# Kernel tuning notes

Measured on AMD Instinct MI355X. Metric: run time of the kernel, lower is better.

The kernel has to match this reference:

```python
import jax, jax.numpy as jnp
import numpy as np

N_NODES = 50000
N_EDGES = 1600000
IN_FEATS = 64
EDGE_INFEAT = 32
HID_FEATS = 128
OUT_FEATS = 4


def setup_inputs() -> dict:
    key = jax.random.key(0)
    ks = jax.random.split(key, 8)
    h = jax.random.normal(ks[0], (N_NODES, IN_FEATS), dtype=jnp.float32)
    edge_feat = jax.random.normal(ks[1], (N_EDGES, EDGE_INFEAT), dtype=jnp.float32)
    src = jax.random.randint(ks[2], (N_EDGES,), 0, N_NODES, dtype=jnp.int32)
    dst = jax.random.randint(ks[3], (N_EDGES,), 0, N_NODES, dtype=jnp.int32)
    cat_dim = 2 * IN_FEATS + EDGE_INFEAT
    # Kaiming-ish scaled weights (nn.Linear default scale ~ 1/sqrt(fan_in))
    W1_w = jax.random.normal(ks[4], (cat_dim, HID_FEATS), dtype=jnp.float32) / np.sqrt(cat_dim)
    W1_b = jax.random.normal(ks[5], (HID_FEATS,), dtype=jnp.float32) * 0.01
    W2_w = jax.random.normal(ks[6], (HID_FEATS, OUT_FEATS), dtype=jnp.float32) / np.sqrt(HID_FEATS)
    W2_b = jax.random.normal(ks[7], (OUT_FEATS,), dtype=jnp.float32) * 0.01
    return {"h": h, "edge_feat": edge_feat, "src": src, "dst": dst,
            "W1_w": W1_w, "W1_b": W1_b, "W2_w": W2_w, "W2_b": W2_b}


def reference(h, edge_feat, src, dst, W1_w, W1_b, W2_w, W2_b):
    # Gather per-edge src/dst node features.  [E, in_feats]
    h_u = jnp.take(h, src, axis=0)
    h_v = jnp.take(h, dst, axis=0)
    # Avoid materializing the [E, 2*in+edge] concat: split the GEMM over the
    # three weight blocks (same math as cat -> Linear).
    Wu = W1_w[:IN_FEATS]            # [in_feats, hid]
    Wv = W1_w[IN_FEATS:2 * IN_FEATS]
    We = W1_w[2 * IN_FEATS:]        # [edge_infeat, hid]
    hid = h_u @ Wu + h_v @ Wv + edge_feat @ We + W1_b  # [E, hid]
    hid = jax.nn.relu(hid)
    return hid @ W2_w + W2_b  # [E, 4]
```

## Files before the change

### kernel.cpp

```cpp
#include <hip/hip_runtime.h>
#include <hip/hip_bf16.h>

#define N_NODES 50000
#define N_EDGES 1600000
#define IN_F 64
#define E_F 32
#define HID 128
#define OUT_F 4

typedef __attribute__((ext_vector_type(4))) float f32x4;
typedef __attribute__((ext_vector_type(8))) short short8;
typedef __attribute__((ext_vector_type(4))) int i32x4;

__device__ inline short f2bf(float f) {
  union { float f; unsigned u; } v; v.f = f;
  unsigned r = v.u + 0x7FFFu + ((v.u >> 16) & 1u);
  return (short)(r >> 16);
}
__device__ inline float bf2f(short s) {
  union { unsigned u; float f; } v; v.u = ((unsigned)(unsigned short)s) << 16;
  return v.f;
}

__global__ __launch_bounds__(256) void node_pre(const float* __restrict__ h,
                                                const float* __restrict__ W1,
                                                short* __restrict__ P) {
  __shared__ float Wl[128 * 128];
  __shared__ float hl[4][64];
  const int tid = threadIdx.x;
  for (int i = tid; i < 128 * 128; i += 256) {
    const int k = i >> 7, j = i & 127;
    Wl[k * 128 + ((j & 15) * 8 + (j >> 4))] = W1[i];
  }

  const int o    = tid & 127;
  const int half = tid >> 7;

  int n0 = blockIdx.x * 98;
  int n1 = min(n0 + 98, N_NODES);
  __syncthreads();

  for (int nb = n0; nb < n1; nb += 4) {
    const int nn = min(4, n1 - nb);
    __syncthreads();
    {
      const int m = tid >> 6, k = tid & 63;
      if (m < nn) hl[m][k] = h[(nb + m) * IN_F + k];
    }
    __syncthreads();
    float acc[4] = {0.f, 0.f, 0.f, 0.f};
#pragma unroll
    for (int k = 0; k < 64; ++k) {
      const float w = Wl[(half * 64 + k) * 128 + o];
#pragma unroll
      for (int m = 0; m < 4; ++m) acc[m] = fmaf(hl[m][k], w, acc[m]);
    }
#pragma unroll
    for (int m = 0; m < 4; ++m)
      if (m < nn) P[(size_t)(nb + m) * 256 + half * 128 + o] = f2bf(acc[m]);
  }
}

#define TPB 8
__global__ __launch_bounds__(256) void edge_mlp(
    const float* __restrict__ ef, const int* __restrict__ src,
    const int* __restrict__ dst, const float* __restrict__ W1,
    const float* __restrict__ b1, const float* __restrict__ W2,
    const float* __restrict__ b2, const short* __restrict__ P,
    float* __restrict__ out) {
  __shared__ __align__(16) short Elds[64 * 32];

  const int tid  = threadIdx.x;
  const int lane = tid & 63;
  const int wid  = tid >> 6;
  const int col  = lane & 15;
  const int rowg = lane >> 4;

  short8 bfrag[8];
#pragma unroll
  for (int t = 0; t < 8; ++t) {
#pragma unroll
    for (int i = 0; i < 8; ++i) {
      const float f = W1[(2 * IN_F + rowg * 8 + i) * HID + t * 16 + col];
      bfrag[t][i] = f2bf(f);
    }
  }
  float b1r[8];
  f32x4 w2r[8];
#pragma unroll
  for (int t = 0; t < 8; ++t) {
    b1r[t] = b1[t * 16 + col];
    w2r[t] = ((const f32x4*)W2)[t * 16 + col];
  }
  const f32x4 b2r = *((const f32x4*)b2);

  for (int tt = 0; tt < TPB; ++tt) {
    const int e0 = (blockIdx.x * TPB + tt) * 64;

    const int ebase = e0 + wid * 16 + rowg * 4;
    const i32x4 se = __builtin_nontemporal_load((const i32x4*)(src + ebase));
    const i32x4 de = __builtin_nontemporal_load((const i32x4*)(dst + ebase));

    const f32x4* efv = (const f32x4*)(ef + (size_t)e0 * E_F);
    const f32x4 a0 = __builtin_nontemporal_load(efv + tid * 2);
    const f32x4 a1 = __builtin_nontemporal_load(efv + tid * 2 + 1);
    short8 pk;
#pragma unroll
    for (int i = 0; i < 4; ++i) pk[i] = f2bf(a0[i]);
#pragma unroll
    for (int i = 0; i < 4; ++i) pk[4 + i] = f2bf(a1[i]);
    __syncthreads();
    ((short8*)Elds)[tid] = pk;
    __syncthreads();

    const short8 af = ((short8*)Elds)[(wid * 16 + col) * 4 + rowg];
    f32x4 acc[8];
#pragma unroll
    for (int t = 0; t < 8; ++t)
      acc[t] = __builtin_amdgcn_mfma_f32_16x16x32_bf16(
          af, bfrag[t], (f32x4){0.f, 0.f, 0.f, 0.f}, 0, 0, 0);

    const int sidx[4] = {se.x, se.y, se.z, se.w};
    const int didx[4] = {de.x, de.y, de.z, de.w};
    short8 lu[4], lv[4];
#pragma unroll
    for (int q = 0; q < 4; ++q) {
      lu[q] = *(const short8*)(P + (size_t)sidx[q] * 256 + col * 8);
      lv[q] = *(const short8*)(P + (size_t)didx[q] * 256 + 128 + col * 8);
    }
    f32x4 part[4] = {(f32x4){0,0,0,0}, (f32x4){0,0,0,0},
                     (f32x4){0,0,0,0}, (f32x4){0,0,0,0}};
#pragma unroll
    for (int q = 0; q < 4; ++q) {
#pragma unroll
      for (int t = 0; t < 8; ++t) {
        float hid = acc[t][q] + bf2f(lu[q][t]) + bf2f(lv[q][t]) + b1r[t];
        hid = fmaxf(hid, 0.f);
#pragma unroll
        for (int o = 0; o < 4; ++o)
          part[q][o] = fmaf(hid, w2r[t][o], part[q][o]);
      }
    }

#pragma unroll
    for (int q = 0; q < 4; ++q) {
#pragma unroll
      for (int o = 0; o < 4; ++o) {
        float v = part[q][o];
        v += __shfl_xor(v, 1);
        v += __shfl_xor(v, 2);
        v += __shfl_xor(v, 4);
        v += __shfl_xor(v, 8);
        part[q][o] = v + b2r[o];
      }
    }
    if (col == 0) {
#pragma unroll
      for (int q = 0; q < 4; ++q)
        __builtin_nontemporal_store(part[q], (f32x4*)out + ebase + q);
    }
  }
}

extern "C" void kernel_launch(void* const* d_in, const int* in_sizes, int n_in,
                              void* d_out, int out_size, void* d_ws, size_t ws_size,
                              hipStream_t stream) {
  const float* h   = (const float*)d_in[0];
  const float* ef  = (const float*)d_in[1];
  const int*   src = (const int*)d_in[2];
  const int*   dst = (const int*)d_in[3];
  const float* W1  = (const float*)d_in[4];
  const float* b1  = (const float*)d_in[5];
  const float* W2  = (const float*)d_in[6];
  const float* b2  = (const float*)d_in[7];
  float* out = (float*)d_out;
  short* P   = (short*)d_ws;

  hipLaunchKernelGGL(node_pre, dim3(512), dim3(256), 0, stream, h, W1, P);
  hipLaunchKernelGGL(edge_mlp, dim3(N_EDGES / (64 * TPB)), dim3(256), 0, stream,
                     ef, src, dst, W1, b1, W2, b2, P, out);
}
```

Baseline: 510.7 us.

## Drop LDS staging in edge and node kernels; load MFMA fragments directly per wave

The edge kernel no longer stages edge features through shared memory with two block barriers per tile. Each wave now owns independent 16-edge tiles and loads its bf16 A-fragment straight from global memory in MFMA layout. The node precompute kernel keeps its weight column in 64 registers instead of LDS, uses more blocks with 49 nodes each, and computes one node at a time. This removes barrier stalls and LDS traffic, at the cost of less coalesced edge-feature loads (32-byte strided rows) and higher register pressure in node_pre.

```diff
diff --git a/kernel.cpp b/kernel.cpp
--- a/kernel.cpp
+++ b/kernel.cpp
@@ -25,51 +25,38 @@
 __global__ __launch_bounds__(256) void node_pre(const float* __restrict__ h,
                                                 const float* __restrict__ W1,
                                                 short* __restrict__ P) {
-  __shared__ float Wl[128 * 128];
-  __shared__ float hl[4][64];
-  const int tid = threadIdx.x;
-  for (int i = tid; i < 128 * 128; i += 256) {
-    const int k = i >> 7, j = i & 127;
-    Wl[k * 128 + ((j & 15) * 8 + (j >> 4))] = W1[i];
-  }
-
+  const int tid  = threadIdx.x;
   const int o    = tid & 127;
   const int half = tid >> 7;
+  const int j    = (o & 7) * 16 + (o >> 3);
 
-  int n0 = blockIdx.x * 98;
-  int n1 = min(n0 + 98, N_NODES);
-  __syncthreads();
+  float wreg[64];
+#pragma unroll
+  for (int k = 0; k < 64; ++k) wreg[k] = W1[(half * 64 + k) * 128 + j];
 
-  for (int nb = n0; nb < n1; nb += 4) {
-    const int nn = min(4, n1 - nb);
-    __syncthreads();
-    {
-      const int m = tid >> 6, k = tid & 63;
-      if (m < nn) hl[m][k] = h[(nb + m) * IN_F + k];
+  const int n0 = blockIdx.x * 49;
+  const int n1 = min(n0 + 49, N_NODES);
+  for (int n = n0; n < n1; ++n) {
+    const float* __restrict__ hrow = h + (size_t)n * IN_F;
+    float a0 = 0.f, a1 = 0.f, a2 = 0.f, a3 = 0.f;
+#pragma unroll
+    for (int k = 0; k < 64; k += 4) {
+      a0 = fmaf(hrow[k    ], wreg[k    ], a0);
+      a1 = fmaf(hrow[k + 1], wreg[k + 1], a1);
+      a2 = fmaf(hrow[k + 2], wreg[k + 2], a2);
+      a3 = fmaf(hrow[k + 3], wreg[k + 3], a3);
     }
-    __syncthreads();
-    float acc[4] = {0.f, 0.f, 0.f, 0.f};
-#pragma unroll
-    for (int k = 0; k < 64; ++k) {
-      const float w = Wl[(half * 64 + k) * 128 + o];
-#pragma unroll
-      for (int m = 0; m < 4; ++m) acc[m] = fmaf(hl[m][k], w, acc[m]);
-    }
-#pragma unroll
-    for (int m = 0; m < 4; ++m)
-      if (m < nn) P[(size_t)(nb + m) * 256 + half * 128 + o] = f2bf(acc[m]);
+    P[(size_t)n * 256 + half * 128 + o] = f2bf((a0 + a1) + (a2 + a3));
   }
 }
 
-#define TPB 8
+#define TPW 8
 __global__ __launch_bounds__(256) void edge_mlp(
     const float* __restrict__ ef, const int* __restrict__ src,
     const int* __restrict__ dst, const float* __restrict__ W1,
     const float* __restrict__ b1, const float* __restrict__ W2,
     const float* __restrict__ b2, const short* __restrict__ P,
     float* __restrict__ out) {
-  __shared__ __align__(16) short Elds[64 * 32];
-
   const int tid  = threadIdx.x;
   const int lane = tid & 63;
   const int wid  = tid >> 6;
@@ -94,26 +81,24 @@
   }
   const f32x4 b2r = *((const f32x4*)b2);
 
-  for (int tt = 0; tt < TPB; ++tt) {
-    const int e0 = (blockIdx.x * TPB + tt) * 64;
+  const int tile0 = (blockIdx.x * 4 + wid) * TPW;
 
-    const int ebase = e0 + wid * 16 + rowg * 4;
+  for (int tt = 0; tt < TPW; ++tt) {
+    const int e0    = (tile0 + tt) * 16;
+    const int ebase = e0 + rowg * 4;
+
     const i32x4 se = __builtin_nontemporal_load((const i32x4*)(src + ebase));
     const i32x4 de = __builtin_nontemporal_load((const i32x4*)(dst + ebase));
 
-    const f32x4* efv = (const f32x4*)(ef + (size_t)e0 * E_F);
-    const f32x4 a0 = __builtin_nontemporal_load(efv + tid * 2);
-    const f32x4 a1 = __builtin_nontemporal_load(efv + tid * 2 + 1);
-    short8 pk;
+    const f32x4* ea = (const f32x4*)(ef + (size_t)(e0 + col) * E_F + rowg * 8);
+    const f32x4 a0 = __builtin_nontemporal_load(ea);
+    const f32x4 a1 = __builtin_nontemporal_load(ea + 1);
+    short8 af;
 #pragma unroll
-    for (int i = 0; i < 4; ++i) pk[i] = f2bf(a0[i]);
+    for (int i = 0; i < 4; ++i) af[i] = f2bf(a0[i]);
 #pragma unroll
-    for (int i = 0; i < 4; ++i) pk[4 + i] = f2bf(a1[i]);
-    __syncthreads();
-    ((short8*)Elds)[tid] = pk;
-    __syncthreads();
+    for (int i = 0; i < 4; ++i) af[4 + i] = f2bf(a1[i]);
 
-    const short8 af = ((short8*)Elds)[(wid * 16 + col) * 4 + rowg];
     f32x4 acc[8];
 #pragma unroll
     for (int t = 0; t < 8; ++t)
@@ -176,7 +161,8 @@
   float* out = (float*)d_out;
   short* P   = (short*)d_ws;
 
-  hipLaunchKernelGGL(node_pre, dim3(512), dim3(256), 0, stream, h, W1, P);
-  hipLaunchKernelGGL(edge_mlp, dim3(N_EDGES / (64 * TPB)), dim3(256), 0, stream,
-                     ef, src, dst, W1, b1, W2, b2, P, out);
+  hipLaunchKernelGGL(node_pre, dim3((N_NODES + 48) / 49), dim3(256), 0, stream,
+                     h, W1, P);
+  hipLaunchKernelGGL(edge_mlp, dim3(N_EDGES / (16 * 4 * TPW)), dim3(256), 0,
+                     stream, ef, src, dst, W1, b1, W2, b2, P, out);
 }
```

After: 514.3 us. No clear change (+0.7%).
